# Kernel tuning notes

Measured on AMD Instinct MI355X. Metric: run time of the kernel, lower is better.

## Reference

```python
import jax, jax.numpy as jnp
import numpy as np

N = 100000
E = 1280000
C = 64
MID = 256
OUT = 64
BN_EPS = 1e-5


def setup_inputs() -> dict:
    key = jax.random.key(0)
    ks = jax.random.split(key, 8)
    x = jax.random.normal(ks[0], (N, C), dtype=jnp.float32)
    edge_index = jax.random.randint(ks[1], (2, E), 0, N, dtype=jnp.int64)
    edge_attr = jax.random.normal(ks[2], (E, 1), dtype=jnp.float32)
    batch = jnp.zeros((N,), dtype=jnp.int64)
    # MLP params: Lin(2C->MID), BatchNorm1d(MID), Lin(MID->OUT)
    W1 = jax.random.normal(ks[3], (2 * C, MID), dtype=jnp.float32) / np.sqrt(2 * C)
    b1 = jnp.zeros((MID,), dtype=jnp.float32)
    gamma = jnp.ones((MID,), dtype=jnp.float32)
    beta = jnp.zeros((MID,), dtype=jnp.float32)
    W2 = jax.random.normal(ks[4], (MID, OUT), dtype=jnp.float32) / np.sqrt(MID)
    b2 = jnp.zeros((OUT,), dtype=jnp.float32)
    return {"x": x, "edge_index": edge_index, "edge_attr": edge_attr, "batch": batch,
            "W1": W1, "b1": b1, "gamma": gamma, "beta": beta, "W2": W2, "b2": b2}


def reference(x, edge_index, edge_attr, batch, W1, b1, gamma, beta, W2, b2):
    n = x.shape[0]
    row, col = edge_index[0], edge_index[1]
    xc = x[col]                                  # [E, C] irregular gather
    feat = jnp.concatenate([xc, xc * edge_attr], axis=1)  # [E, 2C]
    sums = jax.ops.segment_sum(feat, row, num_segments=n)  # [N, 2C]
    cnt = jax.ops.segment_sum(jnp.ones((feat.shape[0],), feat.dtype), row, num_segments=n)
    agg = sums / jnp.maximum(cnt, 1.0)[:, None]  # scatter_mean
    # MLP: Lin -> ReLU -> BatchNorm1d (training stats) -> Lin
    h = jax.nn.relu(agg @ W1 + b1)
    mu = jnp.mean(h, axis=0)
    var = jnp.var(h, axis=0)                     # biased var, as torch BN uses
    h = (h - mu) * jax.lax.rsqrt(var + BN_EPS) * gamma + beta
    return h @ W2 + b2
```

## Files before the change

### kernel.cpp

```cpp
#include <hip/hip_runtime.h>
#include <hip/hip_bf16.h>

#define MIDF 256
#define OUTF 64
#define CF 64
#define TWO_C 128
#define BN_EPS 1e-5f
#define BCAP 1024
#define NBMAX 1600

typedef __attribute__((ext_vector_type(8))) short bf16x8;
typedef __attribute__((ext_vector_type(4))) float f32x4;

__device__ __forceinline__ ushort f2bf(float f) {
  union { float f; unsigned u; } v; v.f = f;
  return (ushort)((v.u + 0x7fffu + ((v.u >> 16) & 1u)) >> 16);
}
__device__ __forceinline__ float bf2f(unsigned u16) {
  union { unsigned u; float f; } v; v.u = u16 << 16;
  return v.f;
}

__global__ __launch_bounds__(1024) void k_init(int* __restrict__ gcur,
                                               float* __restrict__ bnacc, int NB) {
  int i = threadIdx.x;
  for (; i < NB; i += 1024) gcur[i] = i * BCAP;
  i = threadIdx.x;
  if (i < 512) bnacc[i] = 0.f;
}

__global__ __launch_bounds__(1024) void k_front(const int* __restrict__ ei,
    const float* __restrict__ ea, int* __restrict__ gcur, uint2* __restrict__ ebt,
    int E, int NB, int nchunks,
    const float4* __restrict__ xp, uint4* __restrict__ xb, int n8) {
  __shared__ int lh[NBMAX];
  __shared__ int lb[NBMAX];
  int tid = threadIdx.x;
  if ((int)blockIdx.x >= nchunks) {
    int nb2 = gridDim.x - nchunks;
    int i = ((int)blockIdx.x - nchunks) * 1024 + tid;
    int st = nb2 * 1024;
    for (; i < n8; i += st) {
      float4 a = xp[2 * i], b = xp[2 * i + 1];
      uint4 o;
      o.x = (unsigned)f2bf(a.x) | ((unsigned)f2bf(a.y) << 16);
      o.y = (unsigned)f2bf(a.z) | ((unsigned)f2bf(a.w) << 16);
      o.z = (unsigned)f2bf(b.x) | ((unsigned)f2bf(b.y) << 16);
      o.w = (unsigned)f2bf(b.z) | ((unsigned)f2bf(b.w) << 16);
      xb[i] = o;
    }
    return;
  }
  int c0 = blockIdx.x * 4096;
  for (int b = tid; b < NB; b += 1024) lh[b] = 0;
  __syncthreads();
  int rows[4];
#pragma unroll
  for (int j = 0; j < 4; ++j) {
    int e = c0 + j * 1024 + tid;
    int r = (e < E) ? ei[e] : -1;
    rows[j] = r;
    if (r >= 0) atomicAdd(&lh[r >> 6], 1);
  }
  __syncthreads();
  for (int b = tid; b < NB; b += 1024) {
    int c = lh[b];
    lb[b] = (c > 0) ? atomicAdd(&gcur[b], c) : 0;
  }
  __syncthreads();
#pragma unroll
  for (int j = 0; j < 4; ++j) {
    int r = rows[j];
    if (r >= 0) {
      int e = c0 + j * 1024 + tid;
      int pos = atomicAdd(&lb[r >> 6], 1);
      ebt[pos] = make_uint2((unsigned)ei[E + e] | ((unsigned)(r & 63) << 20),
                            __float_as_uint(ea[e]));
    }
  }
}

__global__ __launch_bounds__(512, 4) void k_sortagg(const ushort* __restrict__ xb,
    const uint2* __restrict__ ebt, const int* __restrict__ gcur,
    ushort* __restrict__ agg, int n) {
  __shared__ uint2 recs[BCAP];
  __shared__ int hist[64], cbase[64], cursor[64];
  int tid = threadIdx.x;
  int b = blockIdx.x;
  int base = b * BCAP;
  int cnt = gcur[b] - base;
  if (tid < 64) hist[tid] = 0;
  __syncthreads();
  for (int i = tid; i < cnt; i += 512)
    atomicAdd(&hist[(ebt[base + i].x >> 20) & 63], 1);
  __syncthreads();
  if (tid < 64) {
    int v = hist[tid];
    int sc = v;
#pragma unroll
    for (int d = 1; d < 64; d <<= 1) {
      int t = __shfl_up(sc, d);
      if (tid >= d) sc += t;
    }
    cbase[tid] = sc - v;
    cursor[tid] = sc - v;
  }
  __syncthreads();
  for (int i = tid; i < cnt; i += 512) {
    uint2 rec = ebt[base + i];
    int pos = atomicAdd(&cursor[(rec.x >> 20) & 63], 1);
    recs[pos] = make_uint2(rec.x & 0xFFFFF, rec.y);
  }
  __syncthreads();
  int w = tid >> 6, lane = tid & 63;
  int q4 = lane >> 4, l16 = lane & 15;
#pragma unroll
  for (int j = 0; j < 8; ++j) {
    int rl = w * 8 + j;
    int v = (b << 6) + rl;
    if (v >= n) continue;
    int s = cbase[rl], d = hist[rl];
    int e = s + d;
    float s0 = 0.f, s1 = 0.f, s2 = 0.f, s3 = 0.f;
    float t0 = 0.f, t1 = 0.f, t2 = 0.f, t3 = 0.f;
    int i = s + q4;
    for (; i + 4 < e; i += 8) {
      uint2 pa = recs[i], pb = recs[i + 4];
      uint2 xa = *(const uint2*)(xb + (size_t)pa.x * CF + 4 * l16);
      uint2 xc = *(const uint2*)(xb + (size_t)pb.x * CF + 4 * l16);
      float wa = __uint_as_float(pa.y), wb = __uint_as_float(pb.y);
      float a0 = bf2f(xa.x & 0xffff), a1 = bf2f(xa.x >> 16);
      float a2 = bf2f(xa.y & 0xffff), a3 = bf2f(xa.y >> 16);
      float b0 = bf2f(xc.x & 0xffff), b1 = bf2f(xc.x >> 16);
      float b2 = bf2f(xc.y & 0xffff), b3 = bf2f(xc.y >> 16);
      s0 += a0 + b0; s1 += a1 + b1; s2 += a2 + b2; s3 += a3 + b3;
      t0 += a0 * wa + b0 * wb; t1 += a1 * wa + b1 * wb;
      t2 += a2 * wa + b2 * wb; t3 += a3 * wa + b3 * wb;
    }
    if (i < e) {
      uint2 p = recs[i];
      uint2 xv = *(const uint2*)(xb + (size_t)p.x * CF + 4 * l16);
      float wt = __uint_as_float(p.y);
      float a0 = bf2f(xv.x & 0xffff), a1 = bf2f(xv.x >> 16);
      float a2 = bf2f(xv.y & 0xffff), a3 = bf2f(xv.y >> 16);
      s0 += a0; s1 += a1; s2 += a2; s3 += a3;
      t0 += a0 * wt; t1 += a1 * wt; t2 += a2 * wt; t3 += a3 * wt;
    }
    s0 += __shfl_xor(s0, 16); s1 += __shfl_xor(s1, 16);
    s2 += __shfl_xor(s2, 16); s3 += __shfl_xor(s3, 16);
    t0 += __shfl_xor(t0, 16); t1 += __shfl_xor(t1, 16);
    t2 += __shfl_xor(t2, 16); t3 += __shfl_xor(t3, 16);
    s0 += __shfl_xor(s0, 32); s1 += __shfl_xor(s1, 32);
    s2 += __shfl_xor(s2, 32); s3 += __shfl_xor(s3, 32);
    t0 += __shfl_xor(t0, 32); t1 += __shfl_xor(t1, 32);
    t2 += __shfl_xor(t2, 32); t3 += __shfl_xor(t3, 32);
    float inv = 1.0f / fmaxf((float)d, 1.0f);
    if (q4 == 0) {
      uint2 o;
      o.x = (unsigned)f2bf(s0 * inv) | ((unsigned)f2bf(s1 * inv) << 16);
      o.y = (unsigned)f2bf(s2 * inv) | ((unsigned)f2bf(s3 * inv) << 16);
      *(uint2*)(agg + (size_t)v * TWO_C + 4 * l16) = o;
      uint2 p2;
      p2.x = (unsigned)f2bf(t0 * inv) | ((unsigned)f2bf(t1 * inv) << 16);
      p2.y = (unsigned)f2bf(t2 * inv) | ((unsigned)f2bf(t3 * inv) << 16);
      *(uint2*)(agg + (size_t)v * TWO_C + CF + 4 * l16) = p2;
    }
  }
}

__global__ __launch_bounds__(256, 3) void k_gemm1(const ushort* __restrict__ agg,
    const float* __restrict__ W1, const float* __restrict__ b1,
    ushort* __restrict__ h, float* __restrict__ bnacc, int n, int ntiles) {
  int tid = threadIdx.x, w = tid >> 6, lane = tid & 63;
  int q = lane >> 4, l16 = lane & 15;
  int cg = blockIdx.x & 3;
  int colbase = cg * 64;
  bf16x8 Bf[4][4];
#pragma unroll
  for (int ct = 0; ct < 4; ++ct)
#pragma unroll
    for (int ks = 0; ks < 4; ++ks) {
      int c = colbase + ct * 16 + l16;
      int k0 = ks * 32 + q * 8;
#pragma unroll
      for (int j = 0; j < 8; ++j)
        Bf[ct][ks][j] = (short)f2bf(W1[(size_t)(k0 + j) * MIDF + c]);
    }
  float bias[4];
#pragma unroll
  for (int ct = 0; ct < 4; ++ct) bias[ct] = b1[colbase + ct * 16 + l16];
  __shared__ ushort tile[64 * 72];
  int c_stat = tid & 63, rb = tid >> 6;
  float s_sum = 0.f, s_sq = 0.f;
  int nb = gridDim.x >> 2;
  for (int t = blockIdx.x >> 2; t < ntiles; t += nb) {
    int r0 = t * 64;
    int myrow = r0 + w * 16 + l16;
    bf16x8 Af[4];
#pragma unroll
    for (int ks = 0; ks < 4; ++ks) {
      bf16x8 av;
#pragma unroll
      for (int j = 0; j < 8; ++j) av[j] = 0;
      if (myrow < n) av = *(const bf16x8*)(agg + (size_t)myrow * TWO_C + ks * 32 + q * 8);
      Af[ks] = av;
    }
    f32x4 acc[4];
#pragma unroll
    for (int ct = 0; ct < 4; ++ct) acc[ct] = (f32x4){0.f, 0.f, 0.f, 0.f};
#pragma unroll
    for (int ks = 0; ks < 4; ++ks)
#pragma unroll
      for (int ct = 0; ct < 4; ++ct)
        acc[ct] = __builtin_amdgcn_mfma_f32_16x16x32_bf16(Af[ks], Bf[ct][ks], acc[ct], 0, 0, 0);
    __syncthreads();
#pragma unroll
    for (int ct = 0; ct < 4; ++ct)
#pragma unroll
      for (int r = 0; r < 4; ++r) {
        float vv = fmaxf(acc[ct][r] + bias[ct], 0.f);
        tile[(w * 16 + q * 4 + r) * 72 + ct * 16 + l16] = f2bf(vv);
      }
    __syncthreads();
    int row = tid >> 2, co = (tid & 3) * 16;
    int gr = r0 + row;
    if (gr < n) {
      const uint4* src = (const uint4*)(tile + row * 72 + co);
      uint4* dst = (uint4*)(h + (size_t)gr * MIDF + colbase + co);
      dst[0] = src[0];
      dst[1] = src[1];
    }
#pragma unroll 4
    for (int r = 0; r < 16; ++r) {
      int rr = rb * 16 + r;
      if (r0 + rr < n) {
        float vv = bf2f(tile[rr * 72 + c_stat]);
        s_sum += vv;
        s_sq += vv * vv;
      }
    }
  }
  __syncthreads();
  float* red = (float*)tile;
  red[rb * 64 + c_stat] = s_sum;
  red[256 + rb * 64 + c_stat] = s_sq;
  __syncthreads();
  if (tid < 128) {
    int c = tid & 63, isq = tid >> 6;
    int base = isq * 256;
    float v = red[base + c] + red[base + 64 + c] + red[base + 128 + c] + red[base + 192 + c];
    atomicAdd(&bnacc[isq * MIDF + colbase + c], v);
  }
}

__global__ __launch_bounds__(256) void k_final(const float* __restrict__ bnacc,
    const float* __restrict__ gamma, const float* __restrict__ beta,
    const float* __restrict__ W2, const float* __restrict__ b2,
    float* __restrict__ W2p, float* __restrict__ b2p, float invN) {
  __shared__ float scb[MIDF], shb[MIDF], red[256];
  int tid = threadIdx.x;
  float s = bnacc[tid];
  float q = bnacc[MIDF + tid];
  float mu = s * invN;
  float var = q * invN - mu * mu;
  float sc = gamma[tid] * rsqrtf(var + BN_EPS);
  scb[tid] = sc;
  shb[tid] = beta[tid] - mu * sc;
  __syncthreads();
  float sp = 0.f;
  for (int i = tid; i < MIDF * OUTF; i += 256) {
    int k = i >> 6;
    float wv = W2[i];
    W2p[i] = scb[k] * wv;
    sp += shb[k] * wv;
  }
  red[tid] = sp;
  __syncthreads();
  if (tid < 64)
    b2p[tid] = b2[tid] + red[tid] + red[64 + tid] + red[128 + tid] + red[192 + tid];
}

__global__ __launch_bounds__(256, 2) void k_gemm2(const ushort* __restrict__ h,
    const float* __restrict__ W2p, const float* __restrict__ b2p,
    float* __restrict__ out, int n, int ntiles) {
  int tid = threadIdx.x, w = tid >> 6, lane = tid & 63;
  int q = lane >> 4, l16 = lane & 15;
  bf16x8 Bf[4][8];
#pragma unroll
  for (int ct = 0; ct < 4; ++ct)
#pragma unroll
    for (int ks = 0; ks < 8; ++ks) {
      int c = ct * 16 + l16;
      int k0 = ks * 32 + q * 8;
#pragma unroll
      for (int j = 0; j < 8; ++j)
        Bf[ct][ks][j] = (short)f2bf(W2p[(size_t)(k0 + j) * OUTF + c]);
    }
  float bias[4];
#pragma unroll
  for (int ct = 0; ct < 4; ++ct) bias[ct] = b2p[ct * 16 + l16];
  __shared__ float tile[64 * 68];
  for (int t = blockIdx.x; t < ntiles; t += gridDim.x) {
    int r0 = t * 64;
    int myrow = r0 + w * 16 + l16;
    f32x4 acc[4];
#pragma unroll
    for (int ct = 0; ct < 4; ++ct) acc[ct] = (f32x4){0.f, 0.f, 0.f, 0.f};
#pragma unroll
    for (int ks = 0; ks < 8; ++ks) {
      bf16x8 av;
#pragma unroll
      for (int j = 0; j < 8; ++j) av[j] = 0;
      if (myrow < n) av = *(const bf16x8*)(h + (size_t)myrow * MIDF + ks * 32 + q * 8);
#pragma unroll
      for (int ct = 0; ct < 4; ++ct)
        acc[ct] = __builtin_amdgcn_mfma_f32_16x16x32_bf16(av, Bf[ct][ks], acc[ct], 0, 0, 0);
    }
    __syncthreads();
#pragma unroll
    for (int ct = 0; ct < 4; ++ct)
#pragma unroll
      for (int r = 0; r < 4; ++r)
        tile[(w * 16 + q * 4 + r) * 68 + ct * 16 + l16] = acc[ct][r] + bias[ct];
    __syncthreads();
    int row = tid >> 2, co = (tid & 3) * 16;
    int gr = r0 + row;
    if (gr < n) {
      const float4* src = (const float4*)(tile + row * 68 + co);
      float4* dst = (float4*)(out + (size_t)gr * OUTF + co);
      dst[0] = src[0];
      dst[1] = src[1];
      dst[2] = src[2];
      dst[3] = src[3];
    }
  }
}

extern "C" void kernel_launch(void* const* d_in, const int* in_sizes, int n_in,
                              void* d_out, int out_size, void* d_ws, size_t ws_size,
                              hipStream_t stream) {
  const float* x     = (const float*)d_in[0];
  const int*   ei    = (const int*)d_in[1];
  const float* ea    = (const float*)d_in[2];
  const float* W1    = (const float*)d_in[4];
  const float* b1    = (const float*)d_in[5];
  const float* gamma = (const float*)d_in[6];
  const float* beta  = (const float*)d_in[7];
  const float* W2    = (const float*)d_in[8];
  const float* b2    = (const float*)d_in[9];
  float* out = (float*)d_out;
  int E = in_sizes[2];
  int n = in_sizes[3];
  int NB = (n + 63) >> 6;

  char* ws = (char*)d_ws;
  ushort* agg = (ushort*)ws;
  ushort* h   = agg + (size_t)n * TWO_C;
  ushort* xb  = h + (size_t)n * MIDF;
  float* W2p  = (float*)(xb + (size_t)n * CF);
  float* b2p  = W2p + MIDF * OUTF;
  int* gcur   = (int*)(b2p + 64);
  float* bnacc= (float*)(gcur + NBMAX);
  uint2* ebt  = (uint2*)h;

  int nchunks = (E + 4095) / 4096;
  hipLaunchKernelGGL(k_init, dim3(1), dim3(1024), 0, stream, gcur, bnacc, NB);
  hipLaunchKernelGGL(k_front, dim3(nchunks + 256), dim3(1024), 0, stream,
                     ei, ea, gcur, ebt, E, NB, nchunks,
                     (const float4*)x, (uint4*)xb, n * CF / 8);
  hipLaunchKernelGGL(k_sortagg, dim3(NB), dim3(512), 0, stream, xb, ebt, gcur, agg, n);
  int nt = (n + 63) / 64;
  hipLaunchKernelGGL(k_gemm1, dim3(768), dim3(256), 0, stream, agg, W1, b1, h, bnacc, n, nt);
  hipLaunchKernelGGL(k_final, dim3(1), dim3(256), 0, stream, bnacc, gamma, beta,
                     W2, b2, W2p, b2p, 1.0f / (float)n);
  hipLaunchKernelGGL(k_gemm2, dim3(512), dim3(256), 0, stream, h, W2p, b2p, out, n, nt);
}
```

Baseline: 227.2 us.

## Fuse sort-aggregation with first GEMM via shared-memory aggregate tile

Merges the per-bucket edge sort and mean aggregation with the first linear layer, ReLU and BN statistics into one persistent kernel. The aggregated 64x128 tile stays in LDS and feeds MFMA directly, so the agg intermediate is never written to or read back from global memory. W1 is pre-transposed to bf16 by an extra block in the front kernel, and BN partial sums are spread over four accumulator copies to reduce atomic contention. In exchange, LDS use per block rises substantially, which may lower occupancy. The edge buffer also moves to its own workspace region instead of aliasing h.

```diff
diff --git a/kernel.cpp b/kernel.cpp
--- a/kernel.cpp
+++ b/kernel.cpp
@@ -8,6 +8,8 @@
 #define BN_EPS 1e-5f
 #define BCAP 1024
 #define NBMAX 1600
+#define AGG_LD 136
+#define OB_LD 264
 
 typedef __attribute__((ext_vector_type(8))) short bf16x8;
 typedef __attribute__((ext_vector_type(4))) float f32x4;
@@ -25,19 +27,26 @@
                                                float* __restrict__ bnacc, int NB) {
   int i = threadIdx.x;
   for (; i < NB; i += 1024) gcur[i] = i * BCAP;
-  i = threadIdx.x;
-  if (i < 512) bnacc[i] = 0.f;
+  for (i = threadIdx.x; i < 2048; i += 1024) bnacc[i] = 0.f;
 }
 
 __global__ __launch_bounds__(1024) void k_front(const int* __restrict__ ei,
     const float* __restrict__ ea, int* __restrict__ gcur, uint2* __restrict__ ebt,
     int E, int NB, int nchunks,
-    const float4* __restrict__ xp, uint4* __restrict__ xb, int n8) {
+    const float4* __restrict__ xp, uint4* __restrict__ xb, int n8,
+    const float* __restrict__ W1, ushort* __restrict__ W1t) {
   __shared__ int lh[NBMAX];
   __shared__ int lb[NBMAX];
   int tid = threadIdx.x;
+  if ((int)blockIdx.x == (int)gridDim.x - 1) {
+    for (int i = tid; i < TWO_C * MIDF; i += 1024) {
+      int c = i & (MIDF - 1), k = i >> 8;
+      W1t[(size_t)c * TWO_C + k] = f2bf(W1[(size_t)k * MIDF + c]);
+    }
+    return;
+  }
   if ((int)blockIdx.x >= nchunks) {
-    int nb2 = gridDim.x - nchunks;
+    int nb2 = gridDim.x - 1 - nchunks;
     int i = ((int)blockIdx.x - nchunks) * 1024 + tid;
     int st = nb2 * 1024;
     for (; i < n8; i += st) {
@@ -80,176 +89,175 @@
   }
 }
 
-__global__ __launch_bounds__(512, 4) void k_sortagg(const ushort* __restrict__ xb,
+__global__ __launch_bounds__(512, 4) void k_fused(const ushort* __restrict__ xb,
     const uint2* __restrict__ ebt, const int* __restrict__ gcur,
-    ushort* __restrict__ agg, int n) {
+    const ushort* __restrict__ W1t, const float* __restrict__ b1,
+    ushort* __restrict__ h, float* __restrict__ bnacc, int n, int NB) {
   __shared__ uint2 recs[BCAP];
+  __shared__ ushort aggT[64 * AGG_LD];
+  __shared__ ushort obuf[64 * OB_LD];
   __shared__ int hist[64], cbase[64], cursor[64];
   int tid = threadIdx.x;
-  int b = blockIdx.x;
-  int base = b * BCAP;
-  int cnt = gcur[b] - base;
-  if (tid < 64) hist[tid] = 0;
-  __syncthreads();
-  for (int i = tid; i < cnt; i += 512)
-    atomicAdd(&hist[(ebt[base + i].x >> 20) & 63], 1);
-  __syncthreads();
-  if (tid < 64) {
-    int v = hist[tid];
-    int sc = v;
-#pragma unroll
-    for (int d = 1; d < 64; d <<= 1) {
-      int t = __shfl_up(sc, d);
-      if (tid >= d) sc += t;
-    }
-    cbase[tid] = sc - v;
-    cursor[tid] = sc - v;
-  }
-  __syncthreads();
-  for (int i = tid; i < cnt; i += 512) {
-    uint2 rec = ebt[base + i];
-    int pos = atomicAdd(&cursor[(rec.x >> 20) & 63], 1);
-    recs[pos] = make_uint2(rec.x & 0xFFFFF, rec.y);
-  }
-  __syncthreads();
   int w = tid >> 6, lane = tid & 63;
-  int q4 = lane >> 4, l16 = lane & 15;
-#pragma unroll
-  for (int j = 0; j < 8; ++j) {
-    int rl = w * 8 + j;
-    int v = (b << 6) + rl;
-    if (v >= n) continue;
-    int s = cbase[rl], d = hist[rl];
-    int e = s + d;
-    float s0 = 0.f, s1 = 0.f, s2 = 0.f, s3 = 0.f;
-    float t0 = 0.f, t1 = 0.f, t2 = 0.f, t3 = 0.f;
-    int i = s + q4;
-    for (; i + 4 < e; i += 8) {
-      uint2 pa = recs[i], pb = recs[i + 4];
-      uint2 xa = *(const uint2*)(xb + (size_t)pa.x * CF + 4 * l16);
-      uint2 xc = *(const uint2*)(xb + (size_t)pb.x * CF + 4 * l16);
-      float wa = __uint_as_float(pa.y), wb = __uint_as_float(pb.y);
-      float a0 = bf2f(xa.x & 0xffff), a1 = bf2f(xa.x >> 16);
-      float a2 = bf2f(xa.y & 0xffff), a3 = bf2f(xa.y >> 16);
-      float b0 = bf2f(xc.x & 0xffff), b1 = bf2f(xc.x >> 16);
-      float b2 = bf2f(xc.y & 0xffff), b3 = bf2f(xc.y >> 16);
-      s0 += a0 + b0; s1 += a1 + b1; s2 += a2 + b2; s3 += a3 + b3;
-      t0 += a0 * wa + b0 * wb; t1 += a1 * wa + b1 * wb;
-      t2 += a2 * wa + b2 * wb; t3 += a3 * wa + b3 * wb;
-    }
-    if (i < e) {
-      uint2 p = recs[i];
-      uint2 xv = *(const uint2*)(xb + (size_t)p.x * CF + 4 * l16);
-      float wt = __uint_as_float(p.y);
-      float a0 = bf2f(xv.x & 0xffff), a1 = bf2f(xv.x >> 16);
-      float a2 = bf2f(xv.y & 0xffff), a3 = bf2f(xv.y >> 16);
-      s0 += a0; s1 += a1; s2 += a2; s3 += a3;
-      t0 += a0 * wt; t1 += a1 * wt; t2 += a2 * wt; t3 += a3 * wt;
-    }
-    s0 += __shfl_xor(s0, 16); s1 += __shfl_xor(s1, 16);
-    s2 += __shfl_xor(s2, 16); s3 += __shfl_xor(s3, 16);
-    t0 += __shfl_xor(t0, 16); t1 += __shfl_xor(t1, 16);
-    t2 += __shfl_xor(t2, 16); t3 += __shfl_xor(t3, 16);
-    s0 += __shfl_xor(s0, 32); s1 += __shfl_xor(s1, 32);
-    s2 += __shfl_xor(s2, 32); s3 += __shfl_xor(s3, 32);
-    t0 += __shfl_xor(t0, 32); t1 += __shfl_xor(t1, 32);
-    t2 += __shfl_xor(t2, 32); t3 += __shfl_xor(t3, 32);
-    float inv = 1.0f / fmaxf((float)d, 1.0f);
-    if (q4 == 0) {
-      uint2 o;
-      o.x = (unsigned)f2bf(s0 * inv) | ((unsigned)f2bf(s1 * inv) << 16);
-      o.y = (unsigned)f2bf(s2 * inv) | ((unsigned)f2bf(s3 * inv) << 16);
-      *(uint2*)(agg + (size_t)v * TWO_C + 4 * l16) = o;
-      uint2 p2;
-      p2.x = (unsigned)f2bf(t0 * inv) | ((unsigned)f2bf(t1 * inv) << 16);
-      p2.y = (unsigned)f2bf(t2 * inv) | ((unsigned)f2bf(t3 * inv) << 16);
-      *(uint2*)(agg + (size_t)v * TWO_C + CF + 4 * l16) = p2;
-    }
-  }
-}
-
-__global__ __launch_bounds__(256, 3) void k_gemm1(const ushort* __restrict__ agg,
-    const float* __restrict__ W1, const float* __restrict__ b1,
-    ushort* __restrict__ h, float* __restrict__ bnacc, int n, int ntiles) {
-  int tid = threadIdx.x, w = tid >> 6, lane = tid & 63;
   int q = lane >> 4, l16 = lane & 15;
-  int cg = blockIdx.x & 3;
-  int colbase = cg * 64;
-  bf16x8 Bf[4][4];
-#pragma unroll
-  for (int ct = 0; ct < 4; ++ct)
-#pragma unroll
-    for (int ks = 0; ks < 4; ++ks) {
-      int c = colbase + ct * 16 + l16;
-      int k0 = ks * 32 + q * 8;
-#pragma unroll
-      for (int j = 0; j < 8; ++j)
-        Bf[ct][ks][j] = (short)f2bf(W1[(size_t)(k0 + j) * MIDF + c]);
-    }
-  float bias[4];
-#pragma unroll
-  for (int ct = 0; ct < 4; ++ct) bias[ct] = b1[colbase + ct * 16 + l16];
-  __shared__ ushort tile[64 * 72];
-  int c_stat = tid & 63, rb = tid >> 6;
+  bf16x8 Bf[2][4];
+  float bias[2];
+#pragma unroll
+  for (int c2 = 0; c2 < 2; ++c2) {
+    int col = w * 32 + c2 * 16 + l16;
+#pragma unroll
+    for (int ks = 0; ks < 4; ++ks)
+      Bf[c2][ks] = *(const bf16x8*)(W1t + (size_t)col * TWO_C + ks * 32 + q * 8);
+    bias[c2] = b1[col];
+  }
   float s_sum = 0.f, s_sq = 0.f;
-  int nb = gridDim.x >> 2;
-  for (int t = blockIdx.x >> 2; t < ntiles; t += nb) {
-    int r0 = t * 64;
-    int myrow = r0 + w * 16 + l16;
-    bf16x8 Af[4];
-#pragma unroll
-    for (int ks = 0; ks < 4; ++ks) {
-      bf16x8 av;
-#pragma unroll
-      for (int j = 0; j < 8; ++j) av[j] = 0;
-      if (myrow < n) av = *(const bf16x8*)(agg + (size_t)myrow * TWO_C + ks * 32 + q * 8);
-      Af[ks] = av;
-    }
-    f32x4 acc[4];
-#pragma unroll
-    for (int ct = 0; ct < 4; ++ct) acc[ct] = (f32x4){0.f, 0.f, 0.f, 0.f};
-#pragma unroll
-    for (int ks = 0; ks < 4; ++ks)
-#pragma unroll
-      for (int ct = 0; ct < 4; ++ct)
-        acc[ct] = __builtin_amdgcn_mfma_f32_16x16x32_bf16(Af[ks], Bf[ct][ks], acc[ct], 0, 0, 0);
-    __syncthreads();
-#pragma unroll
-    for (int ct = 0; ct < 4; ++ct)
-#pragma unroll
-      for (int r = 0; r < 4; ++r) {
-        float vv = fmaxf(acc[ct][r] + bias[ct], 0.f);
-        tile[(w * 16 + q * 4 + r) * 72 + ct * 16 + l16] = f2bf(vv);
-      }
-    __syncthreads();
-    int row = tid >> 2, co = (tid & 3) * 16;
-    int gr = r0 + row;
-    if (gr < n) {
-      const uint4* src = (const uint4*)(tile + row * 72 + co);
-      uint4* dst = (uint4*)(h + (size_t)gr * MIDF + colbase + co);
-      dst[0] = src[0];
-      dst[1] = src[1];
+  int c_stat = tid & 255, rb2 = tid >> 8;
+  for (int b = blockIdx.x; b < NB; b += gridDim.x) {
+    int base = b * BCAP;
+    int r0 = b << 6;
+    int cnt = gcur[b] - base;
+    cnt = min(cnt, BCAP);
+    if (tid < 64) hist[tid] = 0;
+    __syncthreads();
+    uint2 e0 = make_uint2(0u, 0u), e1 = make_uint2(0u, 0u);
+    bool v0 = tid < cnt, v1 = 512 + tid < cnt;
+    if (v0) e0 = ebt[base + tid];
+    if (v1) e1 = ebt[base + 512 + tid];
+    if (v0) atomicAdd(&hist[(e0.x >> 20) & 63], 1);
+    if (v1) atomicAdd(&hist[(e1.x >> 20) & 63], 1);
+    __syncthreads();
+    if (tid < 64) {
+      int v = hist[tid];
+      int sc = v;
+#pragma unroll
+      for (int d = 1; d < 64; d <<= 1) {
+        int t = __shfl_up(sc, d);
+        if (tid >= d) sc += t;
+      }
+      cbase[tid] = sc - v;
+      cursor[tid] = sc - v;
+    }
+    __syncthreads();
+    if (v0) {
+      int pos = atomicAdd(&cursor[(e0.x >> 20) & 63], 1);
+      recs[pos] = make_uint2(e0.x & 0xFFFFF, e0.y);
+    }
+    if (v1) {
+      int pos = atomicAdd(&cursor[(e1.x >> 20) & 63], 1);
+      recs[pos] = make_uint2(e1.x & 0xFFFFF, e1.y);
+    }
+    __syncthreads();
+#pragma unroll
+    for (int j = 0; j < 8; ++j) {
+      int rl = w * 8 + j;
+      int s = cbase[rl], d = hist[rl];
+      int e = s + d;
+      float s0 = 0.f, s1 = 0.f, s2 = 0.f, s3 = 0.f;
+      float t0 = 0.f, t1 = 0.f, t2 = 0.f, t3 = 0.f;
+      int i = s + q;
+      for (; i + 4 < e; i += 8) {
+        uint2 pa = recs[i], pb = recs[i + 4];
+        uint2 xa = *(const uint2*)(xb + (size_t)pa.x * CF + 4 * l16);
+        uint2 xc = *(const uint2*)(xb + (size_t)pb.x * CF + 4 * l16);
+        float wa = __uint_as_float(pa.y), wb = __uint_as_float(pb.y);
+        float a0 = bf2f(xa.x & 0xffff), a1 = bf2f(xa.x >> 16);
+        float a2 = bf2f(xa.y & 0xffff), a3 = bf2f(xa.y >> 16);
+        float b0 = bf2f(xc.x & 0xffff), b1v = bf2f(xc.x >> 16);
+        float b2v = bf2f(xc.y & 0xffff), b3 = bf2f(xc.y >> 16);
+        s0 += a0 + b0; s1 += a1 + b1v; s2 += a2 + b2v; s3 += a3 + b3;
+        t0 += a0 * wa + b0 * wb; t1 += a1 * wa + b1v * wb;
+        t2 += a2 * wa + b2v * wb; t3 += a3 * wa + b3 * wb;
+      }
+      if (i < e) {
+        uint2 p = recs[i];
+        uint2 xv = *(const uint2*)(xb + (size_t)p.x * CF + 4 * l16);
+        float wt = __uint_as_float(p.y);
+        float a0 = bf2f(xv.x & 0xffff), a1 = bf2f(xv.x >> 16);
+        float a2 = bf2f(xv.y & 0xffff), a3 = bf2f(xv.y >> 16);
+        s0 += a0; s1 += a1; s2 += a2; s3 += a3;
+        t0 += a0 * wt; t1 += a1 * wt; t2 += a2 * wt; t3 += a3 * wt;
+      }
+      s0 += __shfl_xor(s0, 16); s1 += __shfl_xor(s1, 16);
+      s2 += __shfl_xor(s2, 16); s3 += __shfl_xor(s3, 16);
+      t0 += __shfl_xor(t0, 16); t1 += __shfl_xor(t1, 16);
+      t2 += __shfl_xor(t2, 16); t3 += __shfl_xor(t3, 16);
+      s0 += __shfl_xor(s0, 32); s1 += __shfl_xor(s1, 32);
+      s2 += __shfl_xor(s2, 32); s3 += __shfl_xor(s3, 32);
+      t0 += __shfl_xor(t0, 32); t1 += __shfl_xor(t1, 32);
+      t2 += __shfl_xor(t2, 32); t3 += __shfl_xor(t3, 32);
+      float inv = 1.0f / fmaxf((float)d, 1.0f);
+      if (q == 0) {
+        uint2 o;
+        o.x = (unsigned)f2bf(s0 * inv) | ((unsigned)f2bf(s1 * inv) << 16);
+        o.y = (unsigned)f2bf(s2 * inv) | ((unsigned)f2bf(s3 * inv) << 16);
+        *(uint2*)(aggT + rl * AGG_LD + 4 * l16) = o;
+        uint2 p2;
+        p2.x = (unsigned)f2bf(t0 * inv) | ((unsigned)f2bf(t1 * inv) << 16);
+        p2.y = (unsigned)f2bf(t2 * inv) | ((unsigned)f2bf(t3 * inv) << 16);
+        *(uint2*)(aggT + rl * AGG_LD + CF + 4 * l16) = p2;
+      }
+    }
+    __syncthreads();
+    f32x4 acc[4][2];
+#pragma unroll
+    for (int rt = 0; rt < 4; ++rt)
+#pragma unroll
+      for (int c2 = 0; c2 < 2; ++c2) acc[rt][c2] = (f32x4){0.f, 0.f, 0.f, 0.f};
+#pragma unroll
+    for (int rt = 0; rt < 4; ++rt) {
+      bf16x8 Af[4];
+#pragma unroll
+      for (int ks = 0; ks < 4; ++ks)
+        Af[ks] = *(const bf16x8*)(aggT + (size_t)(rt * 16 + l16) * AGG_LD + ks * 32 + q * 8);
+#pragma unroll
+      for (int ks = 0; ks < 4; ++ks)
+#pragma unroll
+        for (int c2 = 0; c2 < 2; ++c2)
+          acc[rt][c2] = __builtin_amdgcn_mfma_f32_16x16x32_bf16(Af[ks], Bf[c2][ks], acc[rt][c2], 0, 0, 0);
+    }
+#pragma unroll
+    for (int rt = 0; rt < 4; ++rt)
+#pragma unroll
+      for (int c2 = 0; c2 < 2; ++c2)
+#pragma unroll
+        for (int r = 0; r < 4; ++r) {
+          float vv = fmaxf(acc[rt][c2][r] + bias[c2], 0.f);
+          obuf[(rt * 16 + q * 4 + r) * OB_LD + w * 32 + c2 * 16 + l16] = f2bf(vv);
+        }
+    __syncthreads();
+#pragma unroll
+    for (int half = 0; half < 2; ++half) {
+      int row = (tid >> 4) + half * 32;
+      int seg = tid & 15;
+      int gr = r0 + row;
+      if (gr < n) {
+        const uint4* src = (const uint4*)(obuf + row * OB_LD + seg * 16);
+        uint4* dst = (uint4*)(h + (size_t)gr * MIDF + seg * 16);
+        dst[0] = src[0];
+        dst[1] = src[1];
+      }
     }
 #pragma unroll 4
-    for (int r = 0; r < 16; ++r) {
-      int rr = rb * 16 + r;
+    for (int r = 0; r < 32; ++r) {
+      int rr = rb2 * 32 + r;
       if (r0 + rr < n) {
-        float vv = bf2f(tile[rr * 72 + c_stat]);
+        float vv = bf2f(obuf[rr * OB_LD + c_stat]);
         s_sum += vv;
         s_sq += vv * vv;
       }
     }
-  }
-  __syncthreads();
-  float* red = (float*)tile;
-  red[rb * 64 + c_stat] = s_sum;
-  red[256 + rb * 64 + c_stat] = s_sq;
-  __syncthreads();
-  if (tid < 128) {
-    int c = tid & 63, isq = tid >> 6;
-    int base = isq * 256;
-    float v = red[base + c] + red[base + 64 + c] + red[base + 128 + c] + red[base + 192 + c];
-    atomicAdd(&bnacc[isq * MIDF + colbase + c], v);
+    __syncthreads();
+  }
+  float* red = (float*)obuf;
+  red[tid] = s_sum;
+  red[512 + tid] = s_sq;
+  __syncthreads();
+  int cpy = (blockIdx.x & 3) * 512;
+  if (tid < 256) {
+    atomicAdd(&bnacc[cpy + tid], red[tid] + red[256 + tid]);
+  } else {
+    int c = tid - 256;
+    atomicAdd(&bnacc[cpy + 256 + c], red[512 + c] + red[768 + c]);
   }
 }
 
@@ -259,10 +267,10 @@
     float* __restrict__ W2p, float* __restrict__ b2p, float invN) {
   __shared__ float scb[MIDF], shb[MIDF], red[256];
   int tid = threadIdx.x;
-  float s = bnacc[tid];
-  float q = bnacc[MIDF + tid];
+  float s = bnacc[tid] + bnacc[512 + tid] + bnacc[1024 + tid] + bnacc[1536 + tid];
+  float qv = bnacc[256 + tid] + bnacc[768 + tid] + bnacc[1280 + tid] + bnacc[1792 + tid];
   float mu = s * invN;
-  float var = q * invN - mu * mu;
+  float var = qv * invN - mu * mu;
   float sc = gamma[tid] * rsqrtf(var + BN_EPS);
   scb[tid] = sc;
   shb[tid] = beta[tid] - mu * sc;
@@ -354,24 +362,24 @@
   int NB = (n + 63) >> 6;
 
   char* ws = (char*)d_ws;
-  ushort* agg = (ushort*)ws;
-  ushort* h   = agg + (size_t)n * TWO_C;
+  ushort* h   = (ushort*)ws;
   ushort* xb  = h + (size_t)n * MIDF;
-  float* W2p  = (float*)(xb + (size_t)n * CF);
+  uint2* ebt  = (uint2*)(xb + (size_t)n * CF);
+  ushort* W1t = (ushort*)(ebt + (size_t)NBMAX * BCAP);
+  float* W2p  = (float*)(W1t + TWO_C * MIDF);
   float* b2p  = W2p + MIDF * OUTF;
   int* gcur   = (int*)(b2p + 64);
   float* bnacc= (float*)(gcur + NBMAX);
-  uint2* ebt  = (uint2*)h;
 
   int nchunks = (E + 4095) / 4096;
   hipLaunchKernelGGL(k_init, dim3(1), dim3(1024), 0, stream, gcur, bnacc, NB);
-  hipLaunchKernelGGL(k_front, dim3(nchunks + 256), dim3(1024), 0, stream,
+  hipLaunchKernelGGL(k_front, dim3(nchunks + 257), dim3(1024), 0, stream,
                      ei, ea, gcur, ebt, E, NB, nchunks,
-                     (const float4*)x, (uint4*)xb, n * CF / 8);
-  hipLaunchKernelGGL(k_sortagg, dim3(NB), dim3(512), 0, stream, xb, ebt, gcur, agg, n);
-  int nt = (n + 63) / 64;
-  hipLaunchKernelGGL(k_gemm1, dim3(768), dim3(256), 0, stream, agg, W1, b1, h, bnacc, n, nt);
+                     (const float4*)x, (uint4*)xb, n * CF / 8, W1, W1t);
+  hipLaunchKernelGGL(k_fused, dim3(512), dim3(512), 0, stream,
+                     xb, ebt, gcur, W1t, b1, h, bnacc, n, NB);
   hipLaunchKernelGGL(k_final, dim3(1), dim3(256), 0, stream, bnacc, gamma, beta,
                      W2, b2, W2p, b2p, 1.0f / (float)n);
+  int nt = (n + 63) / 64;
   hipLaunchKernelGGL(k_gemm2, dim3(512), dim3(256), 0, stream, h, W2p, b2p, out, n, nt);
 }
```

Result: slower. 249.4 us (+9.8%).
